# Kernel tuning notes

Hardware: AMD Instinct MI355X
Metric: run time of the kernel (lower is better)

The kernel has to match this reference:

```python
import jax, jax.numpy as jnp
import numpy as np

B, L, D, N_LAYERS = 128, 256, 512, 6
NEG = -9e15  # -9000000000000000.0 in the torch source


def _pair_coef(a1, L, D):
    # Faithful reduction of the torch repeat_interleave(dim=2) construction:
    # first half of a_input satisfies a_input[b, i, j, m] = h[b, i, (j*D + m)//L],
    # so sum_m a_input[...,m]*a1[m] = h[b,i] . c[j] with
    # c[j, f] = sum_{m : (j*D+m)//L == f} a1[m].
    j = jnp.arange(L)[:, None]
    m = jnp.arange(D)[None, :]
    idx = (j * D + m) // L  # [L, D], values in [0, D-1]
    c = jnp.zeros((L, D), a1.dtype)
    c = c.at[jnp.arange(L)[:, None], idx].add(jnp.broadcast_to(a1[None, :], (L, D)))
    return c


def gat_layer(x, adj, W, a):
    # h = x @ W; e[b,i,j] = relu(a_input[b,i,j,:] @ a)  (relu overwrites leakyrelu in source)
    h = x @ W  # [B, L, D]
    d = W.shape[1]
    a1, a2 = a[:d, 0], a[d:, 0]
    c = _pair_coef(a1, h.shape[1], d)  # [L, D]
    e = jax.nn.relu(jnp.einsum('bif,jf->bij', h, c) + (h @ a2)[:, None, :])
    att = jnp.where(adj > 0, e, NEG)
    att = jax.nn.softmax(att, axis=2)  # dropout is identity in eval
    h_prime = jnp.einsum('bij,bjd->bid', att, h)
    return jax.nn.elu(h_prime)  # concat=True branch


def position_weight(x, left_len, aspect_len, text_len):
    j = jnp.arange(x.shape[1])[None, :].astype(jnp.float32)  # [1, L]
    l = left_len[:, None].astype(jnp.float32)
    r = (left_len + aspect_len - 1)[:, None].astype(jnp.float32)
    tl = text_len[:, None].astype(jnp.float32)
    ctx = (text_len - aspect_len)[:, None].astype(jnp.float32)
    w = jnp.where(j < l, 1.0 - (l - j) / ctx,
        jnp.where(j <= r, 0.0,
        jnp.where(j < tl, 1.0 - (j - r) / ctx, 0.0)))
    return w[..., None].astype(x.dtype) * x


def aspect_mask(x, left_len, aspect_len):
    j = jnp.arange(x.shape[1])[None, :]
    l = left_len[:, None]
    r = (left_len + aspect_len - 1)[:, None]
    m = ((j >= l) & (j <= r)).astype(x.dtype)
    return m[..., None] * x


def setup_inputs() -> dict:
    key = jax.random.key(0)
    ks = jax.random.split(key, 6)
    x = jax.random.normal(ks[0], (B, L, D), jnp.float32)
    adj = jax.random.randint(ks[1], (B, L, L), 0, 2, jnp.int32)
    adj = adj.at[:, jnp.arange(L), jnp.arange(L)].set(1)  # self loops
    left_len = jax.random.randint(ks[2], (B,), 0, 20, jnp.int32)
    aspect_len = jax.random.randint(ks[3], (B,), 1, 6, jnp.int32)
    text_len = jnp.full((B,), L, jnp.int32)
    W_stack = jax.random.normal(ks[4], (N_LAYERS, D, D), jnp.float32) * (1.414 / np.sqrt(D))
    a_stack = jax.random.normal(ks[5], (N_LAYERS, 2 * D, 1), jnp.float32) * 0.05
    return {"x": x, "W_stack": W_stack, "a_stack": a_stack, "adj": adj,
            "left_len": left_len, "aspect_len": aspect_len, "text_len": text_len}


def reference(x, W_stack, a_stack, adj, left_len, aspect_len, text_len):
    text_out = x
    xp = position_weight(text_out, left_len, aspect_len, text_len)
    h1 = jax.nn.relu(gat_layer(xp, adj, W_stack[0], a_stack[0]))
    h1 = position_weight(h1, left_len, aspect_len, text_len)
    x_graph = jnp.zeros_like(h1)
    for i in range(1, N_LAYERS):
        x_graph = x_graph + jax.nn.relu(gat_layer(h1, adj, W_stack[i], a_stack[i]))
    x_graph = 0.2 * x_graph
    graph_mask = aspect_mask(x_graph, left_len, aspect_len)
    # hop == 1 attention pooling
    alpha_mat = jnp.einsum('bld,bmd->blm', graph_mask, text_out)  # [B, L, L]
    alpha = jax.nn.softmax(alpha_mat.sum(axis=1, keepdims=True), axis=2)  # [B, 1, L]
    a1 = jnp.einsum('blm,bmd->bld', alpha, text_out)[:, 0, :]  # [B, D]
    return a1
```

## Files before the change

### kernel.cpp

```cpp
#include <hip/hip_runtime.h>

#define NB 128
#define NLQ 256
#define ND 512
#define NLAYERS 6
#define DD (ND*ND)
#define MN (1024*ND)
#define HTB 131072

typedef _Float16 f16x8 __attribute__((ext_vector_type(8)));
typedef __fp16 fp16x2 __attribute__((ext_vector_type(2)));
typedef _Float16 f16x4v __attribute__((ext_vector_type(4)));
typedef float f32x4 __attribute__((ext_vector_type(4)));
typedef unsigned int u32x2 __attribute__((ext_vector_type(2)));
typedef unsigned int u32x4 __attribute__((ext_vector_type(4)));
typedef unsigned short ushort_t;

#define GLOAD16(gp, lp) __builtin_amdgcn_global_load_lds( \
    (const __attribute__((address_space(1))) void*)(gp), \
    (__attribute__((address_space(3))) void*)(lp), 16, 0, 0)

__device__ __forceinline__ float wave_max(float v){
  #pragma unroll
  for(int off=32; off; off>>=1) v = fmaxf(v, __shfl_xor(v, off));
  return v;
}
__device__ __forceinline__ float wave_sum(float v){
  #pragma unroll
  for(int off=32; off; off>>=1) v += __shfl_xor(v, off);
  return v;
}
__device__ __forceinline__ unsigned int pk16(float a, float b){
  fp16x2 h = __builtin_amdgcn_cvt_pkrtz(a, b);
  return __builtin_bit_cast(unsigned int, h);
}
__device__ __forceinline__ float f16u(ushort_t u){
  return (float)__builtin_bit_cast(_Float16, u);
}

__global__ __launch_bounds__(256) void k_scal(const float* __restrict__ a_stack,
                                              float* __restrict__ scal){
  int layer = blockIdx.x;
  const float* a = a_stack + (size_t)layer*2*ND;
  int t = threadIdx.x;
  float v0 = a[t];
  float v1 = a[256 + t];
  v0 = wave_sum(v0); v1 = wave_sum(v1);
  __shared__ float s0[4], s1[4];
  int wave = t>>6, lane = t&63;
  if(lane==0){ s0[wave]=v0; s1[wave]=v1; }
  __syncthreads();
  if(t==0){
    scal[layer*2+0] = s0[0]+s0[1]+s0[2]+s0[3];
    scal[layer*2+1] = s1[0]+s1[1]+s1[2]+s1[3];
  }
}

__global__ __launch_bounds__(256) void k_wa2(const float* __restrict__ Wst,
                                             const float* __restrict__ ast,
                                             float* __restrict__ v){
  int l  = blockIdx.x >> 7;
  int rg = blockIdx.x & 127;
  int i  = rg*4 + (threadIdx.x>>6);
  int lane = threadIdx.x & 63;
  const float4* wr = (const float4*)(Wst + (size_t)(l+1)*DD + (size_t)i*ND);
  const float4* ar = (const float4*)(ast + (size_t)(l+1)*2*ND + ND);
  float4 w0=wr[lane], w1=wr[lane+64], a0=ar[lane], a1=ar[lane+64];
  float d = w0.x*a0.x + w0.y*a0.y + w0.z*a0.z + w0.w*a0.w
          + w1.x*a1.x + w1.y*a1.y + w1.z*a1.z + w1.w*a1.w;
  d = wave_sum(d);
  if(lane==0) v[l*ND + i] = d;
}

__global__ __launch_bounds__(256) void k_wcvt(const float* __restrict__ Wsrc,
                                              ushort_t* __restrict__ Ho){
  __shared__ float CT[64][65];
  int bid = blockIdx.x;
  int l  = bid >> 6;
  int kt = (bid >> 3) & 7, nt = bid & 7;
  const float* Wl = Wsrc + (size_t)l*DD;
  int t = threadIdx.x;
  int r = t >> 2, c4 = (t&3)*16;
  #pragma unroll
  for(int u=0;u<4;u++){
    float4 vv = *(const float4*)(Wl + (size_t)(kt*64+r)*ND + nt*64 + c4 + u*4);
    CT[r][c4+u*4+0]=vv.x; CT[r][c4+u*4+1]=vv.y;
    CT[r][c4+u*4+2]=vv.z; CT[r][c4+u*4+3]=vv.w;
  }
  __syncthreads();
  int n = t >> 2, kc = t & 3;
  unsigned int o[8];
  #pragma unroll
  for(int j=0;j<8;j++)
    o[j] = pk16(CT[kc*16 + 2*j][n], CT[kc*16 + 2*j + 1][n]);
  ushort_t* dh = Ho + (size_t)l*DD + (size_t)(nt*64+n)*ND + kt*64 + kc*16;
  *(u32x4*)(dh)     = (u32x4){o[0],o[1],o[2],o[3]};
  *(u32x4*)(dh + 8) = (u32x4){o[4],o[5],o[6],o[7]};
}

__global__ __launch_bounds__(256) void k_xcvt(const float* __restrict__ x,
                                              ushort_t* __restrict__ xp){
  int c = blockIdx.x*256 + threadIdx.x;
  const float4* xr = (const float4*)x;
  float4 v0 = xr[(size_t)c*2], v1 = xr[(size_t)c*2+1];
  u32x4 o = (u32x4){ pk16(v0.x, v0.y), pk16(v0.z, v0.w),
                     pk16(v1.x, v1.y), pk16(v1.z, v1.w) };
  *(u32x4*)(xp + (size_t)c*8) = o;
}

#define BKB 128
template<int MODE>
__device__ __forceinline__ void gemm_tile(const ushort_t* __restrict__ A16,
                                          const ushort_t* __restrict__ Wth,
                                          float* __restrict__ C,
                                          unsigned int* __restrict__ hP,
                                          ushort_t* __restrict__ Pbuf,
                                          float* __restrict__ tp4,
                                          const float* __restrict__ a2,
                                          const float* __restrict__ scal,
                                          const int* __restrict__ left,
                                          const int* __restrict__ asp,
                                          const int* __restrict__ tl,
                                          int mtile, int ntile, unsigned char* lds){
  int t = threadIdx.x;
  int m0 = mtile*128, n0 = ntile*128;
  int lane = t & 63, wid = t >> 6;
  int wr = wid >> 2, wcq = wid & 3;
  int lrow = lane & 15, kb = lane >> 4;

  f32x4 acc[4][2];
  #pragma unroll
  for(int mi=0;mi<4;mi++)
    #pragma unroll
    for(int ni=0;ni<2;ni++)
      acc[mi][ni] = (f32x4){0.f,0.f,0.f,0.f};

  int s_row = t >> 3;
  int s_sl  = (t & 7) ^ (s_row & 7);
  int dstoff = wid*1024;

  const ushort_t* Asrc0 = A16 + (size_t)(m0 + s_row)*ND + s_sl*8;
  const ushort_t* Asrc1 = A16 + (size_t)(m0 + 64 + s_row)*ND + s_sl*8;
  const ushort_t* Bsrc0 = Wth + (size_t)(n0 + s_row)*ND + s_sl*8;
  const ushort_t* Bsrc1 = Wth + (size_t)(n0 + 64 + s_row)*ND + s_sl*8;

  GLOAD16(Asrc0, lds + dstoff);
  GLOAD16(Asrc1, lds + 8192 + dstoff);
  GLOAD16(Bsrc0, lds + 16384 + dstoff);
  GLOAD16(Bsrc1, lds + 24576 + dstoff);
  __syncthreads();

  int cur = 0;
  for(int it=0; it<8; ++it){
    if(it < 7){
      int kn = (it+1)*64;
      unsigned char* dst = lds + ((cur^1)<<15);
      GLOAD16(Asrc0 + kn, dst + dstoff);
      GLOAD16(Asrc1 + kn, dst + 8192 + dstoff);
      GLOAD16(Bsrc0 + kn, dst + 16384 + dstoff);
      GLOAD16(Bsrc1 + kn, dst + 24576 + dstoff);
    }
    unsigned char* Ab = lds + (cur<<15);
    unsigned char* Bb = Ab + 16384;
    #pragma unroll
    for(int ks=0; ks<2; ks++){
      f16x8 ah[4], bh[2];
      #pragma unroll
      for(int mi=0;mi<4;mi++){
        int ar = wr*64 + mi*16 + lrow;
        int sl = (ks*4 + kb) ^ (ar & 7);
        ah[mi] = *(const f16x8*)(Ab + ar*BKB + sl*16);
      }
      #pragma unroll
      for(int ni=0;ni<2;ni++){
        int br = wcq*32 + ni*16 + lrow;
        int sl = (ks*4 + kb) ^ (br & 7);
        bh[ni] = *(const f16x8*)(Bb + br*BKB + sl*16);
      }
      #pragma unroll
      for(int mi=0;mi<4;mi++)
        #pragma unroll
        for(int ni=0;ni<2;ni++)
          acc[mi][ni] = __builtin_amdgcn_mfma_f32_16x16x32_f16(ah[mi], bh[ni], acc[mi][ni], 0,0,0);
    }
    __syncthreads();
    cur ^= 1;
  }

  int rg = lane >> 4;
  int cc = lane & 15;
  if(MODE == 0){
    #pragma unroll
    for(int mi=0;mi<4;mi++)
      #pragma unroll
      for(int ni=0;ni<2;ni++){
        int col = n0 + wcq*32 + ni*16 + cc;
        #pragma unroll
        for(int q=0;q<4;q++){
          int row = m0 + wr*64 + mi*16 + rg*4 + q;
          C[(size_t)row*ND + col] = acc[mi][ni][q];
        }
      }
  } else {
    float S0 = scal[0], S1 = scal[1];
    float* CT = (float*)lds;
    int b = m0 >> 8;
    int ibase = m0 & 255;
    {
      float lf=(float)left[b], aspf=(float)asp[b], tlf=(float)tl[b];
      float rrow=lf+aspf-1.f, inv_ctx=1.f/(tlf-aspf);
      #pragma unroll
      for(int mi=0;mi<4;mi++)
        #pragma unroll
        for(int q=0;q<4;q++){
          float jf = (float)(ibase + wr*64 + mi*16 + rg*4 + q);
          float w;
          if(jf < lf)         w = 1.f-(lf-jf)*inv_ctx;
          else if(jf <= rrow) w = 0.f;
          else if(jf < tlf)   w = 1.f-(jf-rrow)*inv_ctx;
          else                w = 0.f;
          acc[mi][0][q] *= w;
          acc[mi][1][q] *= w;
        }
    }
    int tr   = t >> 2;
    int tch  = t & 3;
    float tpsum = 0.f;
    #pragma unroll
    for(int p=0;p<2;p++){
      if((wcq>>1) == p){
        #pragma unroll
        for(int mi=0;mi<4;mi++)
          #pragma unroll
          for(int ni=0;ni<2;ni++)
            #pragma unroll
            for(int q=0;q<4;q++)
              CT[((wcq&1)*32 + ni*16 + cc)*130 + wr*64 + mi*16 + rg*4 + q] = acc[mi][ni][q];
      }
      __syncthreads();
      int lcol = t >> 6;
      int lrow2 = (t & 63)*2;
      #pragma unroll
      for(int u=0;u<8;u++){
        int c = lcol + u*8;
        float2 v2 = *(float2*)&CT[c*130 + lrow2];
        size_t uidx = ((size_t)b*HTB + (size_t)(n0 + p*64 + c)*256 + ibase + lrow2) >> 1;
        hP[uidx] = pk16(v2.x, v2.y);
      }
      {
        int cpr = t & 31;
        int rq  = t >> 5;
        #pragma unroll
        for(int rr2=0; rr2<8; rr2++){
          int row = rq*8 + rr2;
          float pval = S0*CT[(2*cpr)*130 + row] + S1*CT[(2*cpr+1)*130 + row];
          int ig = ibase + row;
          _Float16 ph = (_Float16)pval;
          size_t addr = (size_t)b*65536 + (size_t)(ig>>5)*8192
                      + (size_t)(ig&31)*256 + (n0>>1) + p*32 + cpr;
          Pbuf[addr] = __builtin_bit_cast(unsigned short, ph);
        }
      }
      #pragma unroll
      for(int cc2=0; cc2<16; cc2++){
        int c = tch*16 + cc2;
        tpsum = fmaf(CT[c*130 + tr], a2[n0 + p*64 + c], tpsum);
      }
      __syncthreads();
    }
    tpsum += __shfl_xor(tpsum, 1);
    tpsum += __shfl_xor(tpsum, 2);
    if(tch == 0) tp4[(n0>>7)*32768 + m0 + tr] = tpsum;
  }
}

__global__ __launch_bounds__(512) void k_gemm_t(const ushort_t* __restrict__ A16,
                                                const ushort_t* __restrict__ Wth,
                                                unsigned int* __restrict__ hP,
                                                ushort_t* __restrict__ Pbuf,
                                                float* __restrict__ tp4,
                                                const float* __restrict__ a2,
                                                const float* __restrict__ scal,
                                                const int* __restrict__ left,
                                                const int* __restrict__ asp,
                                                const int* __restrict__ tl){
  __shared__ unsigned char lds[65536];
  int bid = blockIdx.x;
  int ntile = (bid >> 3) & 3;
  int mtile = (bid & 7) | ((bid >> 5) << 3);
  gemm_tile<1>(A16, Wth, nullptr, hP, Pbuf, tp4, a2, scal, left, asp, tl,
               mtile, ntile, lds);
}

__global__ __launch_bounds__(512) void k_gemm_b(const ushort_t* __restrict__ Abase, long aStride,
                                                const ushort_t* __restrict__ Wth,
                                                float* __restrict__ Cbase){
  __shared__ unsigned char lds[65536];
  int l  = blockIdx.x >> 5;
  int tb = blockIdx.x & 31;
  gemm_tile<0>(Abase + (size_t)l*aStride, Wth + (size_t)l*DD,
               Cbase + (size_t)l*MN, nullptr, nullptr, nullptr,
               nullptr, nullptr, nullptr, nullptr, nullptr, tb>>2, tb&3, lds);
}

__global__ __launch_bounds__(256) void k_attn0(
    const ushort_t* __restrict__ hTH,
    const ushort_t* __restrict__ Pbuf,
    const int* __restrict__ adj,
    const float* __restrict__ tpart,
    const int* __restrict__ left, const int* __restrict__ asp, const int* __restrict__ tl,
    ushort_t* __restrict__ h16){
  __shared__ unsigned char attH[32*512];
  __shared__ unsigned char BsH[16384];

  int bid = blockIdx.x;
  int b  = bid & 127;
  int ic = bid >> 7;
  int i0 = ic*32;
  int tid = threadIdx.x;
  int lane = tid & 63, w = tid >> 6;
  const ushort_t* HH = hTH + (size_t)b*HTB;
  const ushort_t* Pt = Pbuf + (size_t)b*65536 + (size_t)ic*8192;

  float t0v=0.f, t1v=0.f, t2v=0.f, t3v=0.f;
  #pragma unroll
  for(int nt=0; nt<4; nt++){
    float4 tv = ((const float4*)(tpart + nt*32768 + b*256))[lane];
    t0v += tv.x; t1v += tv.y; t2v += tv.z; t3v += tv.w;
  }

  for(int rr=0; rr<8; rr++){
    int il = w*8 + rr;
    int i  = i0 + il;
    f16x4v pv = *(const f16x4v*)(Pt + il*256 + lane*4);
    int4 av = ((const int4*)(adj + ((size_t)b*NLQ + i)*NLQ))[lane];
    float e0 = fmaxf((float)pv[0] + t0v, 0.f);
    float e1 = fmaxf((float)pv[1] + t1v, 0.f);
    float e2 = fmaxf((float)pv[2] + t2v, 0.f);
    float e3 = fmaxf((float)pv[3] + t3v, 0.f);
    float m = -3.0e38f;
    if(av.x>0) m = e0;
    if(av.y>0) m = fmaxf(m, e1);
    if(av.z>0) m = fmaxf(m, e2);
    if(av.w>0) m = fmaxf(m, e3);
    m = wave_max(m);
    float p0 = (av.x>0) ? __expf(e0-m) : 0.f;
    float p1 = (av.y>0) ? __expf(e1-m) : 0.f;
    float p2 = (av.z>0) ? __expf(e2-m) : 0.f;
    float p3 = (av.w>0) ? __expf(e3-m) : 0.f;
    float s = wave_sum(p0+p1+p2+p3);
    float inv = 1.f/s;
    unsigned int w0 = pk16(p0*inv, p1*inv);
    unsigned int w1 = pk16(p2*inv, p3*inv);
    int off = il*512 + ((lane*8) ^ ((il&7)<<4));
    *(u32x2*)(attH + off) = (u32x2){w0,w1};
  }

  int wm = w >> 1, wn = w & 1;
  int lrow = lane & 15, kb = lane >> 4;
  int rg = lane >> 4, cc = lane & 15;
  float lf=(float)left[b], aspf=(float)asp[b], tlf=(float)tl[b];
  float rrv=lf+aspf-1.f, ctx=tlf-aspf;
  int arow = wm*16 + lrow;
  int aswz = (arow&7)<<4;

  for(int dp=0; dp<2; dp++){
    int d0 = dp*256;
    f32x4 acc[8];
    #pragma unroll
    for(int ni=0;ni<8;ni++) acc[ni] = (f32x4){0.f,0.f,0.f,0.f};
    for(int ks=0; ks<8; ks++){
      int j0 = ks*32;
      __syncthreads();
      #pragma unroll
      for(int u=0;u<4;u++){
        int chunk = (u*4 + w)*64 + lane;
        int row = chunk >> 2, sl = chunk & 3;
        GLOAD16(HH + (size_t)(d0+row)*256 + j0 + sl*8, BsH + (u*4+w)*1024);
      }
      __syncthreads();
      int aoff = arow*512 + ((j0*2 + kb*16) ^ aswz);
      f16x8 ah = *(const f16x8*)(attH + aoff);
      #pragma unroll
      for(int ni=0; ni<8; ni++){
        f16x8 bh = *(const f16x8*)(BsH + (wn*128 + ni*16 + lrow)*64 + kb*16);
        acc[ni] = __builtin_amdgcn_mfma_f32_16x16x32_f16(ah, bh, acc[ni], 0,0,0);
      }
    }
    #pragma unroll
    for(int q=0;q<4;q++){
      int row = i0 + wm*16 + rg*4 + q;
      float fi = (float)row;
      float wgt;
      if(fi < lf)        wgt = 1.f-(lf-fi)/ctx;
      else if(fi <= rrv) wgt = 0.f;
      else if(fi < tlf)  wgt = 1.f-(fi-rrv)/ctx;
      else               wgt = 0.f;
      #pragma unroll
      for(int ni=0;ni<8;ni++){
        int col = d0 + wn*128 + ni*16 + cc;
        float ov = wgt*fmaxf(acc[ni][q], 0.f);
        h16[((size_t)b*NLQ + row)*ND + col] =
            __builtin_bit_cast(unsigned short, (_Float16)ov);
      }
    }
  }
}

__global__ __launch_bounds__(256) void k_tv(const ushort_t* __restrict__ h16,
                                            const float* __restrict__ v,
                                            float* __restrict__ T){
  int row  = blockIdx.x*4 + (threadIdx.x>>6);
  int lane = threadIdx.x & 63;
  f16x8 hv = *(const f16x8*)(h16 + (size_t)row*ND + lane*8);
  float hf[8];
  #pragma unroll
  for(int i=0;i<8;i++) hf[i] = (float)hv[i];
  float s0,s1,s2,s3,s4;
  #define DOTV(SL, L) { \
    const float4* vr = (const float4*)(v + (L)*ND); \
    float4 v0 = vr[lane*2], v1 = vr[lane*2+1]; \
    float dd = hf[0]*v0.x+hf[1]*v0.y+hf[2]*v0.z+hf[3]*v0.w \
             + hf[4]*v1.x+hf[5]*v1.y+hf[6]*v1.z+hf[7]*v1.w; \
    SL = wave_sum(dd); }
  DOTV(s0,0) DOTV(s1,1) DOTV(s2,2) DOTV(s3,3) DOTV(s4,4)
  #undef DOTV
  if(lane==0){
    T[0*32768 + row]=s0; T[1*32768 + row]=s1; T[2*32768 + row]=s2;
    T[3*32768 + row]=s3; T[4*32768 + row]=s4;
  }
}

__global__ __launch_bounds__(256) void k_rows(const ushort_t* __restrict__ h16,
                                              const int* __restrict__ left, const int* __restrict__ asp,
                                              ushort_t* __restrict__ R){
  int b = blockIdx.x;
  int nk = asp[b], l0 = left[b];
  const unsigned int* src = (const unsigned int*)(h16 + (size_t)b*NLQ*ND);
  unsigned int* dst = (unsigned int*)(R + (size_t)b*8*ND);
  #pragma unroll
  for(int u=0; u<8; u++){
    int idx = threadIdx.x + u*256;
    int k = idx >> 8, c = idx & 255;
    dst[idx] = (k<nk) ? src[(size_t)(l0+k)*256 + c] : 0u;
  }
}

__global__ __launch_bounds__(256) void k_att5(const ushort_t* __restrict__ h16,
    const float* __restrict__ Hasp, const float* __restrict__ T,
    const int* __restrict__ adj, const float* __restrict__ scal,
    const int* __restrict__ left, const int* __restrict__ asp,
    ushort_t* __restrict__ y){
  __shared__ float att[5][260];
  int b  = blockIdx.x & 127;
  int l  = blockIdx.x >> 7;
  int tid = threadIdx.x, lane = tid&63, w = tid>>6;
  int nk = asp[b], l0 = left[b];
  float S0 = scal[2*(l+1)], S1 = scal[2*(l+1)+1];

  for(int k = w; k < 5; k += 4){
    if(k < nk){
      const float2* hrow = (const float2*)(Hasp + (size_t)l*MN + (size_t)(b*8+k)*ND);
      const int* arow = adj + ((size_t)b*NLQ + (l0+k))*NLQ;
      const float* Tl = T + l*32768 + b*256;
      float e[4]; int av[4];
      float m = -3.0e38f;
      #pragma unroll
      for(int q=0;q<4;q++){
        int j = lane + 64*q;
        float2 hp = hrow[j];
        av[q] = arow[j];
        e[q] = fmaxf(S0*hp.x + S1*hp.y + Tl[j], 0.f);
        if(av[q] > 0) m = fmaxf(m, e[q]);
      }
      m = wave_max(m);
      float pp[4]; float s = 0.f;
      #pragma unroll
      for(int q=0;q<4;q++){
        pp[q] = (av[q] > 0) ? __expf(e[q]-m) : 0.f;
        s += pp[q];
      }
      s = wave_sum(s);
      float inv = 1.f/s;
      #pragma unroll
      for(int q=0;q<4;q++) att[k][lane+64*q] = pp[q]*inv;
    } else {
      #pragma unroll
      for(int q=0;q<4;q++) att[k][lane+64*q] = 0.f;
    }
  }
  __syncthreads();

  int d = tid;
  const ushort_t* hb = h16 + (size_t)b*NLQ*ND;
  float ax[5] = {0,0,0,0,0}, ay[5] = {0,0,0,0,0};
  for(int jj=0; jj<NLQ; jj++){
    float hx = f16u(hb[(size_t)jj*ND + d]);
    float hy = f16u(hb[(size_t)jj*ND + 256 + d]);
    #pragma unroll
    for(int k=0;k<5;k++){
      float a = att[k][jj];
      ax[k] += a*hx;
      ay[k] += a*hy;
    }
  }
  ushort_t* yb = y + (size_t)l*MN + (size_t)b*8*ND;
  #pragma unroll
  for(int k=0;k<5;k++){
    yb[(size_t)k*ND + d]       = __builtin_bit_cast(unsigned short, (_Float16)ax[k]);
    yb[(size_t)k*ND + 256 + d] = __builtin_bit_cast(unsigned short, (_Float16)ay[k]);
  }
  #pragma unroll
  for(int u=0;u<6;u++) yb[5*ND + u*256 + tid] = 0;
}

__global__ __launch_bounds__(256) void k_g(const float* __restrict__ hp,
    const int* __restrict__ asp, float* __restrict__ g){
  int b = blockIdx.x, d = threadIdx.x;
  int nk = asp[b];
  float gx=0.f, gy=0.f;
  for(int l=0;l<5;l++){
    for(int k=0;k<nk;k++){
      const float* r = hp + (size_t)l*MN + (size_t)(b*8+k)*ND;
      gx += fmaxf(r[d], 0.f);
      gy += fmaxf(r[d+256], 0.f);
    }
  }
  g[b*ND + d]       = 0.2f*gx;
  g[b*ND + 256 + d] = 0.2f*gy;
}

__global__ __launch_bounds__(256) void k_dot(const ushort_t* __restrict__ x16,
    const float* __restrict__ g, float* __restrict__ s){
  int row  = blockIdx.x*4 + (threadIdx.x>>6);
  int b    = row >> 8;
  int lane = threadIdx.x & 63;
  f16x8 xv = *(const f16x8*)(x16 + (size_t)row*ND + lane*8);
  const float4* gr = (const float4*)(g + (size_t)b*ND);
  float4 g0 = gr[lane*2], g1 = gr[lane*2+1];
  float d = (float)xv[0]*g0.x + (float)xv[1]*g0.y + (float)xv[2]*g0.z + (float)xv[3]*g0.w
          + (float)xv[4]*g1.x + (float)xv[5]*g1.y + (float)xv[6]*g1.z + (float)xv[7]*g1.w;
  d = wave_sum(d);
  if(lane==0) s[row] = d;
}

__global__ __launch_bounds__(256) void k_out(const ushort_t* __restrict__ x16,
    const float* __restrict__ s, float* __restrict__ out){
  int b  = blockIdx.x >> 2;
  int ch = blockIdx.x & 3;
  int tid = threadIdx.x, lane = tid&63, w = tid>>6;
  __shared__ float red[4];
  __shared__ float alpha[NLQ];
  __shared__ float part[128];
  float sv = s[b*NLQ + tid];
  float m = wave_max(sv);
  if(lane==0) red[w] = m;
  __syncthreads();
  m = fmaxf(fmaxf(red[0],red[1]), fmaxf(red[2],red[3]));
  float p = __expf(sv - m);
  float su = wave_sum(p);
  __syncthreads();
  if(lane==0) red[w] = su;
  __syncthreads();
  su = red[0]+red[1]+red[2]+red[3];
  alpha[tid] = p/su;
  __syncthreads();
  int d = ch*128 + (tid & 127);
  int half = tid >> 7;
  const ushort_t* xb = x16 + (size_t)b*NLQ*ND;
  float acc = 0.f;
  for(int mm = half*128; mm < half*128 + 128; mm++)
    acc += alpha[mm] * f16u(xb[(size_t)mm*ND + d]);
  if(half) part[tid & 127] = acc;
  __syncthreads();
  if(!half) out[(size_t)b*ND + d] = acc + part[tid & 127];
}

extern "C" void kernel_launch(void* const* d_in, const int* in_sizes, int n_in,
                              void* d_out, int out_size, void* d_ws, size_t ws_size,
                              hipStream_t stream){
  const float* x    = (const float*)d_in[0];
  const float* Wst  = (const float*)d_in[1];
  const float* ast  = (const float*)d_in[2];
  const int*   adj  = (const int*)d_in[3];
  const int*   left = (const int*)d_in[4];
  const int*   asp  = (const int*)d_in[5];
  const int*   tl   = (const int*)d_in[6];
  float* out = (float*)d_out;
  float* ws  = (float*)d_ws;

  const size_t SZ = (size_t)NB*NLQ*ND;
  float* bufA = ws;
  float* bufB = ws + SZ;
  float* ws2  = ws + 2*SZ;
  float* tpart= ws2;
  float* T    = tpart + 4*32768;
  float* g    = T + 163840;
  float* scal = g + 65536;
  float* v    = scal + 16;
  float* sbuf = v + 2560;
  ushort_t* w0th = (ushort_t*)(sbuf + 32768);

  ushort_t* Pbuf = (ushort_t*)bufA;
  ushort_t* h16  = Pbuf + (size_t)NB*65536;

  ushort_t* hTH  = (ushort_t*)bufB;
  ushort_t* x16  = (ushort_t*)(bufB + (SZ>>1));

  float* Hasp = bufB;
  ushort_t* y16 = (ushort_t*)(Hasp + (size_t)5*MN);
  float* hp   = (float*)(y16 + (size_t)5*MN);
  {
  }
  float* hpF  = bufB + (size_t)5*MN + (size_t)5*MN/2;
  ushort_t* R16 = (ushort_t*)(hpF + (size_t)5*MN);
  ushort_t* wt15h = (ushort_t*)((float*)R16 + (size_t)MN/2);

  k_scal<<<NLAYERS, 256, 0, stream>>>(ast, scal);
  k_wa2<<<5*128, 256, 0, stream>>>(Wst, ast, v);
  k_wcvt<<<64, 256, 0, stream>>>(Wst, w0th);
  k_xcvt<<<8192, 256, 0, stream>>>(x, x16);

  k_gemm_t<<<(NB*NLQ/128)*(ND/128), 512, 0, stream>>>(x16, w0th,
      (unsigned int*)hTH, Pbuf, tpart, ast + ND, scal, left, asp, tl);
  k_attn0<<<NB*8, 256, 0, stream>>>(hTH, Pbuf, adj, tpart, left, asp, tl, h16);

  k_wcvt<<<5*64, 256, 0, stream>>>(Wst + DD, wt15h);
  k_tv<<<NB*NLQ/4, 256, 0, stream>>>(h16, v, T);
  k_rows<<<NB, 256, 0, stream>>>(h16, left, asp, R16);
  k_gemm_b<<<5*32, 512, 0, stream>>>(R16, 0L, wt15h, Hasp);
  k_att5<<<5*NB, 256, 0, stream>>>(h16, Hasp, T, adj, scal, left, asp, y16);
  k_gemm_b<<<5*32, 512, 0, stream>>>(y16, (long)MN, wt15h, hpF);
  k_g<<<NB, 256, 0, stream>>>(hpF, asp, g);

  k_dot<<<NB*NLQ/4, 256, 0, stream>>>(x16, g, sbuf);
  k_out<<<NB*4, 256, 0, stream>>>(x16, sbuf, out);
}
```

Measured before the change: 213.2 us.

## Merge prep kernels into one launch and double-buffer attn0 B-tile loads

Result: no change. 210.8 us (-1.1%).

```diff
diff --git a/kernel.cpp b/kernel.cpp
--- a/kernel.cpp
+++ b/kernel.cpp
@@ -38,69 +38,75 @@
   return (float)__builtin_bit_cast(_Float16, u);
 }
 
-__global__ __launch_bounds__(256) void k_scal(const float* __restrict__ a_stack,
-                                              float* __restrict__ scal){
-  int layer = blockIdx.x;
-  const float* a = a_stack + (size_t)layer*2*ND;
-  int t = threadIdx.x;
-  float v0 = a[t];
-  float v1 = a[256 + t];
-  v0 = wave_sum(v0); v1 = wave_sum(v1);
-  __shared__ float s0[4], s1[4];
-  int wave = t>>6, lane = t&63;
-  if(lane==0){ s0[wave]=v0; s1[wave]=v1; }
-  __syncthreads();
-  if(t==0){
-    scal[layer*2+0] = s0[0]+s0[1]+s0[2]+s0[3];
-    scal[layer*2+1] = s1[0]+s1[1]+s1[2]+s1[3];
-  }
-}
-
-__global__ __launch_bounds__(256) void k_wa2(const float* __restrict__ Wst,
-                                             const float* __restrict__ ast,
-                                             float* __restrict__ v){
-  int l  = blockIdx.x >> 7;
-  int rg = blockIdx.x & 127;
-  int i  = rg*4 + (threadIdx.x>>6);
-  int lane = threadIdx.x & 63;
-  const float4* wr = (const float4*)(Wst + (size_t)(l+1)*DD + (size_t)i*ND);
-  const float4* ar = (const float4*)(ast + (size_t)(l+1)*2*ND + ND);
-  float4 w0=wr[lane], w1=wr[lane+64], a0=ar[lane], a1=ar[lane+64];
-  float d = w0.x*a0.x + w0.y*a0.y + w0.z*a0.z + w0.w*a0.w
-          + w1.x*a1.x + w1.y*a1.y + w1.z*a1.z + w1.w*a1.w;
-  d = wave_sum(d);
-  if(lane==0) v[l*ND + i] = d;
-}
-
-__global__ __launch_bounds__(256) void k_wcvt(const float* __restrict__ Wsrc,
-                                              ushort_t* __restrict__ Ho){
+__global__ __launch_bounds__(256) void k_prep(const float* __restrict__ Wst,
+                                              const float* __restrict__ ast,
+                                              const float* __restrict__ x,
+                                              float* __restrict__ scal,
+                                              float* __restrict__ v,
+                                              ushort_t* __restrict__ w0th,
+                                              ushort_t* __restrict__ wt15h,
+                                              ushort_t* __restrict__ xp){
   __shared__ float CT[64][65];
   int bid = blockIdx.x;
-  int l  = bid >> 6;
-  int kt = (bid >> 3) & 7, nt = bid & 7;
-  const float* Wl = Wsrc + (size_t)l*DD;
   int t = threadIdx.x;
-  int r = t >> 2, c4 = (t&3)*16;
-  #pragma unroll
-  for(int u=0;u<4;u++){
-    float4 vv = *(const float4*)(Wl + (size_t)(kt*64+r)*ND + nt*64 + c4 + u*4);
-    CT[r][c4+u*4+0]=vv.x; CT[r][c4+u*4+1]=vv.y;
-    CT[r][c4+u*4+2]=vv.z; CT[r][c4+u*4+3]=vv.w;
-  }
-  __syncthreads();
-  int n = t >> 2, kc = t & 3;
-  unsigned int o[8];
-  #pragma unroll
-  for(int j=0;j<8;j++)
-    o[j] = pk16(CT[kc*16 + 2*j][n], CT[kc*16 + 2*j + 1][n]);
-  ushort_t* dh = Ho + (size_t)l*DD + (size_t)(nt*64+n)*ND + kt*64 + kc*16;
-  *(u32x4*)(dh)     = (u32x4){o[0],o[1],o[2],o[3]};
-  *(u32x4*)(dh + 8) = (u32x4){o[4],o[5],o[6],o[7]};
-}
-
-__global__ __launch_bounds__(256) void k_xcvt(const float* __restrict__ x,
-                                              ushort_t* __restrict__ xp){
-  int c = blockIdx.x*256 + threadIdx.x;
+  if(bid < 6){
+    int layer = bid;
+    const float* a = ast + (size_t)layer*2*ND;
+    float v0 = a[t];
+    float v1 = a[256 + t];
+    v0 = wave_sum(v0); v1 = wave_sum(v1);
+    float* s0 = &CT[0][0];
+    float* s1 = &CT[1][0];
+    int wave = t>>6, lane = t&63;
+    if(lane==0){ s0[wave]=v0; s1[wave]=v1; }
+    __syncthreads();
+    if(t==0){
+      scal[layer*2+0] = s0[0]+s0[1]+s0[2]+s0[3];
+      scal[layer*2+1] = s1[0]+s1[1]+s1[2]+s1[3];
+    }
+    return;
+  }
+  if(bid < 646){
+    int b2 = bid - 6;
+    int l  = b2 >> 7;
+    int rg = b2 & 127;
+    int i  = rg*4 + (t>>6);
+    int lane = t & 63;
+    const float4* wr = (const float4*)(Wst + (size_t)(l+1)*DD + (size_t)i*ND);
+    const float4* ar = (const float4*)(ast + (size_t)(l+1)*2*ND + ND);
+    float4 w0=wr[lane], w1=wr[lane+64], a0=ar[lane], a1=ar[lane+64];
+    float d = w0.x*a0.x + w0.y*a0.y + w0.z*a0.z + w0.w*a0.w
+            + w1.x*a1.x + w1.y*a1.y + w1.z*a1.z + w1.w*a1.w;
+    d = wave_sum(d);
+    if(lane==0) v[l*ND + i] = d;
+    return;
+  }
+  if(bid < 1030){
+    const float* Wsrc; ushort_t* Ho; int b3;
+    if(bid < 710){ Wsrc = Wst;      Ho = w0th;  b3 = bid - 646; }
+    else         { Wsrc = Wst + DD; Ho = wt15h; b3 = bid - 710; }
+    int l  = b3 >> 6;
+    int kt = (b3 >> 3) & 7, nt = b3 & 7;
+    const float* Wl = Wsrc + (size_t)l*DD;
+    int r = t >> 2, c4 = (t&3)*16;
+    #pragma unroll
+    for(int u=0;u<4;u++){
+      float4 vv = *(const float4*)(Wl + (size_t)(kt*64+r)*ND + nt*64 + c4 + u*4);
+      CT[r][c4+u*4+0]=vv.x; CT[r][c4+u*4+1]=vv.y;
+      CT[r][c4+u*4+2]=vv.z; CT[r][c4+u*4+3]=vv.w;
+    }
+    __syncthreads();
+    int n = t >> 2, kc = t & 3;
+    unsigned int o[8];
+    #pragma unroll
+    for(int j=0;j<8;j++)
+      o[j] = pk16(CT[kc*16 + 2*j][n], CT[kc*16 + 2*j + 1][n]);
+    ushort_t* dh = Ho + (size_t)l*DD + (size_t)(nt*64+n)*ND + kt*64 + kc*16;
+    *(u32x4*)(dh)     = (u32x4){o[0],o[1],o[2],o[3]};
+    *(u32x4*)(dh + 8) = (u32x4){o[4],o[5],o[6],o[7]};
+    return;
+  }
+  int c = (bid - 1030)*256 + t;
   const float4* xr = (const float4*)x;
   float4 v0 = xr[(size_t)c*2], v1 = xr[(size_t)c*2+1];
   u32x4 o = (u32x4){ pk16(v0.x, v0.y), pk16(v0.z, v0.w),
@@ -311,7 +317,7 @@
     const int* __restrict__ left, const int* __restrict__ asp, const int* __restrict__ tl,
     ushort_t* __restrict__ h16){
   __shared__ unsigned char attH[32*512];
-  __shared__ unsigned char BsH[16384];
+  __shared__ unsigned char BsH[2][16384];
 
   int bid = blockIdx.x;
   int b  = bid & 127;
@@ -364,28 +370,45 @@
   int arow = wm*16 + lrow;
   int aswz = (arow&7)<<4;
 
+  {
+    #pragma unroll
+    for(int u=0;u<4;u++){
+      int chunk = (u*4 + w)*64 + lane;
+      int row = chunk >> 2, sl = chunk & 3;
+      GLOAD16(HH + (size_t)row*256 + sl*8, BsH[0] + (u*4+w)*1024);
+    }
+  }
+  __syncthreads();
+
+  int tt = 0;
   for(int dp=0; dp<2; dp++){
     int d0 = dp*256;
     f32x4 acc[8];
     #pragma unroll
     for(int ni=0;ni<8;ni++) acc[ni] = (f32x4){0.f,0.f,0.f,0.f};
     for(int ks=0; ks<8; ks++){
+      if(tt < 15){
+        int nt2 = tt + 1;
+        int dpp = nt2 >> 3, kss = nt2 & 7;
+        int dn = dpp*256, jn = kss*32;
+        #pragma unroll
+        for(int u=0;u<4;u++){
+          int chunk = (u*4 + w)*64 + lane;
+          int row = chunk >> 2, sl = chunk & 3;
+          GLOAD16(HH + (size_t)(dn+row)*256 + jn + sl*8, BsH[nt2&1] + (u*4+w)*1024);
+        }
+      }
       int j0 = ks*32;
-      __syncthreads();
-      #pragma unroll
-      for(int u=0;u<4;u++){
-        int chunk = (u*4 + w)*64 + lane;
-        int row = chunk >> 2, sl = chunk & 3;
-        GLOAD16(HH + (size_t)(d0+row)*256 + j0 + sl*8, BsH + (u*4+w)*1024);
-      }
-      __syncthreads();
+      const unsigned char* Bb = BsH[tt&1];
       int aoff = arow*512 + ((j0*2 + kb*16) ^ aswz);
       f16x8 ah = *(const f16x8*)(attH + aoff);
       #pragma unroll
       for(int ni=0; ni<8; ni++){
-        f16x8 bh = *(const f16x8*)(BsH + (wn*128 + ni*16 + lrow)*64 + kb*16);
+        f16x8 bh = *(const f16x8*)(Bb + (wn*128 + ni*16 + lrow)*64 + kb*16);
         acc[ni] = __builtin_amdgcn_mfma_f32_16x16x32_f16(ah, bh, acc[ni], 0,0,0);
       }
+      __syncthreads();
+      tt++;
     }
     #pragma unroll
     for(int q=0;q<4;q++){
@@ -603,29 +626,22 @@
 
   ushort_t* Pbuf = (ushort_t*)bufA;
   ushort_t* h16  = Pbuf + (size_t)NB*65536;
+  ushort_t* wt15h = h16 + (size_t)NB*NLQ*ND;
 
   ushort_t* hTH  = (ushort_t*)bufB;
   ushort_t* x16  = (ushort_t*)(bufB + (SZ>>1));
 
   float* Hasp = bufB;
   ushort_t* y16 = (ushort_t*)(Hasp + (size_t)5*MN);
-  float* hp   = (float*)(y16 + (size_t)5*MN);
-  {
-  }
   float* hpF  = bufB + (size_t)5*MN + (size_t)5*MN/2;
   ushort_t* R16 = (ushort_t*)(hpF + (size_t)5*MN);
-  ushort_t* wt15h = (ushort_t*)((float*)R16 + (size_t)MN/2);
-
-  k_scal<<<NLAYERS, 256, 0, stream>>>(ast, scal);
-  k_wa2<<<5*128, 256, 0, stream>>>(Wst, ast, v);
-  k_wcvt<<<64, 256, 0, stream>>>(Wst, w0th);
-  k_xcvt<<<8192, 256, 0, stream>>>(x, x16);
+
+  k_prep<<<9222, 256, 0, stream>>>(Wst, ast, x, scal, v, w0th, wt15h, x16);
 
   k_gemm_t<<<(NB*NLQ/128)*(ND/128), 512, 0, stream>>>(x16, w0th,
       (unsigned int*)hTH, Pbuf, tpart, ast + ND, scal, left, asp, tl);
   k_attn0<<<NB*8, 256, 0, stream>>>(hTH, Pbuf, adj, tpart, left, asp, tl, h16);
 
-  k_wcvt<<<5*64, 256, 0, stream>>>(Wst + DD, wt15h);
   k_tv<<<NB*NLQ/4, 256, 0, stream>>>(h16, v, T);
   k_rows<<<NB, 256, 0, stream>>>(h16, left, asp, R16);
   k_gemm_b<<<5*32, 512, 0, stream>>>(R16, 0L, wt15h, Hasp);
```
